# Kernel tuning notes

Measured on AMD Instinct MI355X. Metric: run time of the kernel, lower is better.

The kernel has to match this reference:

```python
import jax, jax.numpy as jnp
import numpy as np

FEATURE_SIZE = 128
STRIDE = 16
BASE_SIZE = 16
RATIOS = [0.5, 1, 2]
SCALES = [8, 16, 32]


def _generate_anchors(feature_size, stride):
    # Faithful to the torch module's numpy anchor generation (incl. rounding).
    size = BASE_SIZE * BASE_SIZE
    size_ratios = size / np.array(RATIOS)
    ws = np.round(np.sqrt(size_ratios))
    hs = np.round(ws * np.array(RATIOS))
    base = []
    for w, h in zip(ws, hs):
        for s in SCALES:
            base.append([0.0, 0.0, w * s, h * s])
    base = np.array(base)  # [9, 4]
    xo, yo = np.meshgrid(np.arange(feature_size), np.arange(feature_size), indexing='ij')
    # original loop order: x outer, y inner, then 9 base anchors
    centers = np.stack([xo * stride, yo * stride], axis=-1).reshape(-1, 1, 2)  # [F*F,1,2]
    wh = np.broadcast_to(base[None, :, 2:4], (feature_size * feature_size, 9, 2))
    anchors = np.concatenate([np.broadcast_to(centers, wh.shape), wh], axis=-1).reshape(-1, 4)
    return jnp.asarray(anchors, dtype=jnp.float32)  # [F*F*9, 4]


def _conv(x, w, b, pad):
    y = jax.lax.conv_general_dilated(
        x, w, window_strides=(1, 1), padding=[(pad, pad), (pad, pad)],
        dimension_numbers=('NCHW', 'OIHW', 'NCHW'))
    return y + b[None, :, None, None]


def setup_inputs() -> dict:
    key = jax.random.key(0)
    ks = jax.random.split(key, 4)
    F = FEATURE_SIZE
    x = jax.random.normal(ks[0], (1, 1024, F, F), dtype=jnp.float32)
    base_w = jax.random.normal(ks[1], (512, 1024, 3, 3), dtype=jnp.float32) * 0.01
    base_b = jnp.zeros((512,), dtype=jnp.float32)
    cls_w = jax.random.normal(ks[2], (18, 512, 1, 1), dtype=jnp.float32) * 0.01
    cls_b = jnp.zeros((18,), dtype=jnp.float32)
    reg_w = jax.random.normal(ks[3], (36, 512, 1, 1), dtype=jnp.float32) * 0.01
    reg_b = jnp.zeros((36,), dtype=jnp.float32)
    return {"x": x, "base_w": base_w, "base_b": base_b,
            "cls_w": cls_w, "cls_b": cls_b, "reg_w": reg_w, "reg_b": reg_b}


def reference(x, base_w, base_b, cls_w, cls_b, reg_w, reg_b):
    F = FEATURE_SIZE
    anchors = _generate_anchors(F, STRIDE)  # [N,4], N = F*F*9

    rpn_conv = jax.nn.relu(_conv(x, base_w, base_b, pad=1))        # [1,512,F,F]
    rpn_cls = _conv(rpn_conv, cls_w, cls_b, pad=0)                  # [1,18,F,F]
    # softmax over the 2-way fg/bg axis after reshape, as in the original
    cls_rs = rpn_cls.reshape(1, 2, 9 * F, F)
    cls_prob = jax.nn.softmax(cls_rs, axis=1).reshape(1, 18, F, F)
    rpn_reg = _conv(rpn_conv, reg_w, reg_b, pad=0)                  # [1,36,F,F]

    cls = jnp.transpose(cls_prob, (0, 2, 3, 1)).reshape(-1, 2)      # [N,2]
    reg = jnp.transpose(rpn_reg, (0, 2, 3, 1)).reshape(-1, 4)       # [N,4]

    # Vectorized decode — faithful to the original per-anchor loop math:
    # p0 = ax + aw*d0 ; p1 = ay + ah*d1 ; p2 = aw + exp(d2) ; p3 = ah + exp(d3)
    p0 = anchors[:, 0] + anchors[:, 2] * reg[:, 0]
    p1 = anchors[:, 1] + anchors[:, 3] * reg[:, 1]
    p2 = anchors[:, 2] + jnp.exp(reg[:, 2])
    p3 = anchors[:, 3] + jnp.exp(reg[:, 3])
    proposals = jnp.stack([p0, p1, p2, p3], axis=-1)                # [N,4]
    scores = cls[:, 1]                                              # [N]
    return jnp.concatenate([proposals, scores[:, None]], axis=-1)   # [N,5]
```

## Files before the change

kernel.cpp:

```cpp
#include <hip/hip_runtime.h>
#include <hip/hip_bf16.h>

typedef unsigned short u16;
typedef short s8v __attribute__((ext_vector_type(8)));
typedef float f4v __attribute__((ext_vector_type(4)));

#define F 128
#define CIN 1024
#define CMID 512
#define XP 130
#define K9 9216
#define BK 64

__device__ __forceinline__ u16 f2bf(float v) {
    union { float f; unsigned u; } x; x.f = v;
    unsigned r = x.u + 0x7fff + ((x.u >> 16) & 1);
    return (u16)(r >> 16);
}
__device__ __forceinline__ float bf2f(u16 u) {
    union { unsigned u; float f; } x; x.u = ((unsigned)u) << 16; return x.f;
}

__device__ __forceinline__ void gl16(const u16* g, u16* l) {
    __builtin_amdgcn_global_load_lds(
        (const __attribute__((address_space(1))) void*)g,
        (__attribute__((address_space(3))) void*)l,
        16, 0, 0);
}

__constant__ float WBASE[9] = {184.f, 368.f, 736.f, 128.f, 256.f, 512.f,  88.f, 176.f, 352.f};
__constant__ float HBASE[9] = { 96.f, 192.f, 384.f, 128.f, 256.f, 512.f, 176.f, 352.f, 704.f};

__global__ void prep_border(u16* __restrict__ xpad) {
    int t = blockIdx.x * 256 + threadIdx.x;
    if (t >= 516 * 1024) return;
    int c = t & 1023;
    int cell = t >> 10;
    int h, w;
    if (cell < 130)      { h = 0;   w = cell; }
    else if (cell < 260) { h = 129; w = cell - 130; }
    else { int rm = cell - 260; h = 1 + (rm >> 1); w = (rm & 1) * 129; }
    xpad[(h * XP + w) * CIN + c] = 0;
}

__global__ void prep_xpad(const float* __restrict__ x, u16* __restrict__ xpad) {
    __shared__ float lds[64][65];
    const int h  = blockIdx.x;
    const int w0 = blockIdx.y * 64;
    const int c0 = blockIdx.z * 64;
    const int tid = threadIdx.x;
    {
        const int wl = tid & 63, ci = tid >> 6;
        #pragma unroll
        for (int k = 0; k < 16; ++k) {
            int cl = ci * 16 + k;
            lds[cl][wl] = x[(c0 + cl) * (F * F) + h * F + (w0 + wl)];
        }
    }
    __syncthreads();
    {
        const int cs = (tid & 7) * 8;
        #pragma unroll
        for (int pass = 0; pass < 2; ++pass) {
            const int wl = (tid >> 3) + pass * 32;
            s8v v;
            #pragma unroll
            for (int j = 0; j < 8; ++j) v[j] = (short)f2bf(lds[cs + j][wl]);
            *(s8v*)&xpad[((h + 1) * XP + (w0 + wl + 1)) * CIN + c0 + cs] = v;
        }
    }
}

__global__ void prep_wt(const float* __restrict__ bw, u16* __restrict__ wt) {
    __shared__ u16 lds[K9];
    const int oc = blockIdx.x;
    const int tid = threadIdx.x;
    for (int k = 0; k < 36; ++k) {
        int idx = k * 256 + tid;
        float v = bw[oc * K9 + idx];
        int c = idx / 9, q = idx - c * 9;
        lds[q * CIN + c] = f2bf(v);
    }
    __syncthreads();
    for (int k = 0; k < 36; ++k) {
        int idx = k * 256 + tid;
        wt[oc * K9 + idx] = lds[idx];
    }
}

__global__ void prep_wc(const float* __restrict__ cls_w, const float* __restrict__ reg_w,
                        u16* __restrict__ wc) {
    int t = blockIdx.x * 256 + threadIdx.x;
    int oc = t >> 9, c = t & 511;
    float v = 0.f;
    if (oc < 18)      v = cls_w[oc * 512 + c];
    else if (oc < 54) v = reg_w[(oc - 18) * 512 + c];
    wc[t] = f2bf(v);
}

__global__ __launch_bounds__(256, 2) void gemm_conv(
    const u16* __restrict__ xpad, const u16* __restrict__ wt,
    const float* __restrict__ bias, u16* __restrict__ rpn) {
    __shared__ u16 smem[4 * 128 * BK];
    const int tid = threadIdx.x;
    const int gh  = blockIdx.x;
    const int oc0 = blockIdx.y * 128;

    const int lane = tid & 63;
    const int wv = tid >> 6;
    const int lm = lane & 15;
    const int lq = lane >> 4;
    const int wm = (wv >> 1) * 64;
    const int wn = (wv & 1) * 64;

    const u16* pa[4];
    const u16* pb[4];
    #pragma unroll
    for (int j = 0; j < 4; ++j) {
        int r = wv * 32 + j * 8 + (lane >> 3);
        int s8 = ((lane & 7) ^ (r & 7)) * 8;
        pa[j] = xpad + r * CIN + s8;
        pb[j] = wt + (size_t)(oc0 + r) * K9 + s8;
    }

    f4v acc[4][4] = {};

    auto issue = [&](int step, int buf) {
        const int dydx = step >> 4;
        const int cc   = step & 15;
        const int dy = dydx / 3, dx = dydx - dy * 3;
        const int aoff = ((gh + dy) * XP + dx) * CIN + cc * 64;
        const int boff = dydx * CIN + cc * 64;
        u16* Ab = smem + (buf * 2 + 0) * (128 * BK) + (wv * 32) * BK;
        u16* Bb = smem + (buf * 2 + 1) * (128 * BK) + (wv * 32) * BK;
        #pragma unroll
        for (int j = 0; j < 4; ++j) {
            gl16(pa[j] + aoff, Ab + j * 8 * BK);
            gl16(pb[j] + boff, Bb + j * 8 * BK);
        }
    };

    issue(0, 0);
    __syncthreads();
    for (int step = 0; step < 144; ++step) {
        const int buf = step & 1;
        if (step + 1 < 144) issue(step + 1, buf ^ 1);
        const u16* Ab = smem + (buf * 2 + 0) * (128 * BK);
        const u16* Bb = smem + (buf * 2 + 1) * (128 * BK);
        #pragma unroll
        for (int kk = 0; kk < 2; ++kk) {
            s8v af[4], bfr[4];
            #pragma unroll
            for (int i = 0; i < 4; ++i) {
                int ra = wm + i * 16 + lm;
                int rb = wn + i * 16 + lm;
                af[i]  = *(const s8v*)&Ab[ra * BK + (((kk * 4 + lq) ^ (ra & 7)) * 8)];
                bfr[i] = *(const s8v*)&Bb[rb * BK + (((kk * 4 + lq) ^ (rb & 7)) * 8)];
            }
            #pragma unroll
            for (int mi = 0; mi < 4; ++mi)
                #pragma unroll
                for (int ni = 0; ni < 4; ++ni)
                    acc[mi][ni] = __builtin_amdgcn_mfma_f32_16x16x32_bf16(
                        af[mi], bfr[ni], acc[mi][ni], 0, 0, 0);
        }
        __syncthreads();
    }

    #pragma unroll
    for (int ni = 0; ni < 4; ++ni) {
        const int oc = oc0 + wn + ni * 16 + lm;
        const float b = bias[oc];
        #pragma unroll
        for (int mi = 0; mi < 4; ++mi) {
            #pragma unroll
            for (int rr = 0; rr < 4; ++rr) {
                const int m = wm + mi * 16 + lq * 4 + rr;
                float v = acc[mi][ni][rr] + b;
                v = v > 0.f ? v : 0.f;
                rpn[(gh * 128 + m) * CMID + oc] = f2bf(v);
            }
        }
    }
}

__global__ __launch_bounds__(256) void stage2(
    const u16* __restrict__ rpn, const u16* __restrict__ wc,
    const float* __restrict__ cls_b, const float* __restrict__ reg_b,
    float* __restrict__ vals) {
    const int tid = threadIdx.x, lane = tid & 63, wv = tid >> 6;
    const int lm = lane & 15, lq = lane >> 4;
    const int m0 = blockIdx.x * 64 + wv * 16;
    f4v acc[4] = {};
    const u16* arow = rpn + (m0 + lm) * CMID + lq * 8;
    const u16* brow = wc + lm * CMID + lq * 8;
    #pragma unroll
    for (int k = 0; k < 16; ++k) {
        s8v af = *(const s8v*)(arow + k * 32);
        #pragma unroll
        for (int ni = 0; ni < 4; ++ni) {
            s8v bf = *(const s8v*)(brow + ni * 16 * CMID + k * 32);
            acc[ni] = __builtin_amdgcn_mfma_f32_16x16x32_bf16(af, bf, acc[ni], 0, 0, 0);
        }
    }
    #pragma unroll
    for (int ni = 0; ni < 4; ++ni) {
        const int ch = ni * 16 + lm;
        const float b = ch < 18 ? cls_b[ch] : (ch < 54 ? reg_b[ch - 18] : 0.f);
        #pragma unroll
        for (int rr = 0; rr < 4; ++rr)
            vals[(m0 + lq * 4 + rr) * 64 + ch] = acc[ni][rr] + b;
    }
}

__global__ void stage3(const float* __restrict__ vals, float* __restrict__ out) {
    const int t = blockIdx.x * 256 + threadIdx.x;
    const int p = t / 9, a = t - p * 9;
    const float* v = vals + p * 64;
    const int ch = 2 * a + 1;
    const int pair = (ch < 9) ? ch + 9 : ch - 9;
    const float score = 1.f / (1.f + expf(v[pair] - v[ch]));
    const float r0 = v[18 + 4 * a], r1 = v[19 + 4 * a];
    const float r2 = v[20 + 4 * a], r3 = v[21 + 4 * a];
    const float wb = WBASE[a], hb = HBASE[a];
    const int h = p >> 7, w = p & 127;
    float* o = out + t * 5;
    o[0] = h * 16.f + wb * r0;
    o[1] = w * 16.f + hb * r1;
    o[2] = wb + expf(r2);
    o[3] = hb + expf(r3);
    o[4] = score;
}

extern "C" void kernel_launch(void* const* d_in, const int* in_sizes, int n_in,
                              void* d_out, int out_size, void* d_ws, size_t ws_size,
                              hipStream_t stream) {
    const float* x      = (const float*)d_in[0];
    const float* base_w = (const float*)d_in[1];
    const float* base_b = (const float*)d_in[2];
    const float* cls_w  = (const float*)d_in[3];
    const float* cls_b  = (const float*)d_in[4];
    const float* reg_w  = (const float*)d_in[5];
    const float* reg_b  = (const float*)d_in[6];
    float* out = (float*)d_out;

    char* ws = (char*)d_ws;
    u16*  xpad = (u16*)ws;
    u16*  wt   = (u16*)(ws + 34611200);
    u16*  wc   = (u16*)(ws + 34611200 + 9437184);
    u16*  rpn  = (u16*)(ws + 34611200 + 9437184 + 65536);
    float* vals = (float*)(ws + 34611200 + 9437184 + 65536 + 16777216);

    prep_border<<<2064, 256, 0, stream>>>(xpad);
    prep_xpad<<<dim3(128, 2, 16), 256, 0, stream>>>(x, xpad);
    prep_wt<<<512, 256, 0, stream>>>(base_w, wt);
    prep_wc<<<128, 256, 0, stream>>>(cls_w, reg_w, wc);
    gemm_conv<<<dim3(128, 4), 256, 0, stream>>>(xpad, wt, base_b, rpn);
    stage2<<<256, 256, 0, stream>>>(rpn, wc, cls_b, reg_b, vals);
    stage3<<<576, 256, 0, stream>>>(vals, out);
}
```

Measured before the change: 278.7 us.

## Merge prep kernels, share A tile across dx taps, fuse stage2 and stage3

Merges the four preprocessing kernels into a single launch, with vectorized border zeroing and a padded LDS stride for the weight transpose. The conv GEMM now loads a 130-row A tile once per (dy, channel-chunk) and reuses it for all three dx taps by shifting row indices, so only B is reloaded per step. Block indices are remapped so that neighbouring rows and output-channel tiles run close together, which may improve L2 reuse. The 1x1 conv and decode stages are fused through shared memory, which removes the intermediate vals buffer and one launch. The cost is a more complex pipeline with an extra sync per dx step and slightly more LDS use.

```diff
diff --git a/kernel.cpp b/kernel.cpp
--- a/kernel.cpp
+++ b/kernel.cpp
@@ -10,7 +10,11 @@
 #define CMID 512
 #define XP 130
 #define K9 9216
-#define BK 64
+
+#define A_ELEMS 8704
+#define B_ELEMS 8192
+#define AOFF(b) ((b) * A_ELEMS)
+#define BOFF(b) (2 * A_ELEMS + (b) * B_ELEMS)
 
 __device__ __forceinline__ u16 f2bf(float v) {
     union { float f; unsigned u; } x; x.f = v;
@@ -31,80 +35,82 @@
 __constant__ float WBASE[9] = {184.f, 368.f, 736.f, 128.f, 256.f, 512.f,  88.f, 176.f, 352.f};
 __constant__ float HBASE[9] = { 96.f, 192.f, 384.f, 128.f, 256.f, 512.f, 176.f, 352.f, 704.f};
 
-__global__ void prep_border(u16* __restrict__ xpad) {
-    int t = blockIdx.x * 256 + threadIdx.x;
-    if (t >= 516 * 1024) return;
-    int c = t & 1023;
-    int cell = t >> 10;
-    int h, w;
-    if (cell < 130)      { h = 0;   w = cell; }
-    else if (cell < 260) { h = 129; w = cell - 130; }
-    else { int rm = cell - 260; h = 1 + (rm >> 1); w = (rm & 1) * 129; }
-    xpad[(h * XP + w) * CIN + c] = 0;
-}
-
-__global__ void prep_xpad(const float* __restrict__ x, u16* __restrict__ xpad) {
-    __shared__ float lds[64][65];
-    const int h  = blockIdx.x;
-    const int w0 = blockIdx.y * 64;
-    const int c0 = blockIdx.z * 64;
+__global__ __launch_bounds__(256) void prep_all(
+    const float* __restrict__ x, const float* __restrict__ bw,
+    const float* __restrict__ cls_w, const float* __restrict__ reg_w,
+    u16* __restrict__ xpad, u16* __restrict__ wt, u16* __restrict__ wc) {
+    __shared__ char ldsraw[18624];
+    const int b = blockIdx.x;
     const int tid = threadIdx.x;
-    {
-        const int wl = tid & 63, ci = tid >> 6;
-        #pragma unroll
-        for (int k = 0; k < 16; ++k) {
-            int cl = ci * 16 + k;
-            lds[cl][wl] = x[(c0 + cl) * (F * F) + h * F + (w0 + wl)];
-        }
-    }
-    __syncthreads();
-    {
-        const int cs = (tid & 7) * 8;
-        #pragma unroll
-        for (int pass = 0; pass < 2; ++pass) {
-            const int wl = (tid >> 3) + pass * 32;
-            s8v v;
-            #pragma unroll
-            for (int j = 0; j < 8; ++j) v[j] = (short)f2bf(lds[cs + j][wl]);
-            *(s8v*)&xpad[((h + 1) * XP + (w0 + wl + 1)) * CIN + c0 + cs] = v;
-        }
-    }
-}
-
-__global__ void prep_wt(const float* __restrict__ bw, u16* __restrict__ wt) {
-    __shared__ u16 lds[K9];
-    const int oc = blockIdx.x;
-    const int tid = threadIdx.x;
-    for (int k = 0; k < 36; ++k) {
-        int idx = k * 256 + tid;
-        float v = bw[oc * K9 + idx];
-        int c = idx / 9, q = idx - c * 9;
-        lds[q * CIN + c] = f2bf(v);
-    }
-    __syncthreads();
-    for (int k = 0; k < 36; ++k) {
-        int idx = k * 256 + tid;
-        wt[oc * K9 + idx] = lds[idx];
-    }
-}
-
-__global__ void prep_wc(const float* __restrict__ cls_w, const float* __restrict__ reg_w,
-                        u16* __restrict__ wc) {
-    int t = blockIdx.x * 256 + threadIdx.x;
-    int oc = t >> 9, c = t & 511;
-    float v = 0.f;
-    if (oc < 18)      v = cls_w[oc * 512 + c];
-    else if (oc < 54) v = reg_w[(oc - 18) * 512 + c];
-    wc[t] = f2bf(v);
+
+    if (b < 258) {
+        int t = b * 256 + tid;
+        int cell = t >> 7, c8 = (t & 127) * 8;
+        int h, w;
+        if (cell < 130)      { h = 0;   w = cell; }
+        else if (cell < 260) { h = 129; w = cell - 130; }
+        else { int rm = cell - 260; h = 1 + (rm >> 1); w = (rm & 1) * 129; }
+        s8v z = {};
+        *(s8v*)&xpad[(h * XP + w) * CIN + c8] = z;
+    } else if (b < 4354) {
+        float (*lds)[65] = (float(*)[65])ldsraw;
+        const int b2 = b - 258;
+        const int h  = b2 >> 5;
+        const int w0 = ((b2 >> 4) & 1) * 64;
+        const int c0 = (b2 & 15) * 64;
+        {
+            const int wl = tid & 63, ci = tid >> 6;
+            #pragma unroll
+            for (int k = 0; k < 16; ++k) {
+                int cl = ci * 16 + k;
+                lds[cl][wl] = x[(c0 + cl) * (F * F) + h * F + (w0 + wl)];
+            }
+        }
+        __syncthreads();
+        {
+            const int cs = (tid & 7) * 8;
+            #pragma unroll
+            for (int pass = 0; pass < 2; ++pass) {
+                const int wl = (tid >> 3) + pass * 32;
+                s8v v;
+                #pragma unroll
+                for (int j = 0; j < 8; ++j) v[j] = (short)f2bf(lds[cs + j][wl]);
+                *(s8v*)&xpad[((h + 1) * XP + (w0 + wl + 1)) * CIN + c0 + cs] = v;
+            }
+        }
+    } else if (b < 4866) {
+        u16* lds = (u16*)ldsraw;
+        const int oc = b - 4354;
+        for (int k = 0; k < 36; ++k) {
+            int idx = k * 256 + tid;
+            float v = bw[oc * K9 + idx];
+            int c = idx / 9, q = idx - c * 9;
+            lds[q * 1033 + c] = f2bf(v);
+        }
+        __syncthreads();
+        for (int k = 0; k < 36; ++k) {
+            int idx = k * 256 + tid;
+            int q = idx >> 10, c = idx & 1023;
+            wt[oc * K9 + idx] = lds[q * 1033 + c];
+        }
+    } else {
+        int t = (b - 4866) * 256 + tid;
+        int oc = t >> 9, c = t & 511;
+        float v = 0.f;
+        if (oc < 18)      v = cls_w[oc * 512 + c];
+        else if (oc < 54) v = reg_w[(oc - 18) * 512 + c];
+        wc[t] = f2bf(v);
+    }
 }
 
 __global__ __launch_bounds__(256, 2) void gemm_conv(
     const u16* __restrict__ xpad, const u16* __restrict__ wt,
     const float* __restrict__ bias, u16* __restrict__ rpn) {
-    __shared__ u16 smem[4 * 128 * BK];
+    __shared__ u16 smem[2 * A_ELEMS + 2 * B_ELEMS];
     const int tid = threadIdx.x;
-    const int gh  = blockIdx.x;
-    const int oc0 = blockIdx.y * 128;
+    const int bid = blockIdx.x;
+    const int oc0 = ((bid & 7) >> 1) * 128;
+    const int gh  = (bid >> 3) * 2 + (bid & 1);
 
     const int lane = tid & 63;
     const int wv = tid >> 6;
@@ -113,70 +119,81 @@
     const int wm = (wv >> 1) * 64;
     const int wn = (wv & 1) * 64;
 
-    const u16* pa[4];
-    const u16* pb[4];
-    #pragma unroll
-    for (int j = 0; j < 4; ++j) {
-        int r = wv * 32 + j * 8 + (lane >> 3);
-        int s8 = ((lane & 7) ^ (r & 7)) * 8;
-        pa[j] = xpad + r * CIN + s8;
-        pb[j] = wt + (size_t)(oc0 + r) * K9 + s8;
-    }
+    const int sw = (lane & 7) ^ ((lane >> 3) & 7);
+    const u16* pA = xpad + (lane >> 3) * CIN + sw * 8;
+    const u16* pB = wt + (size_t)(oc0 + wv * 32 + (lane >> 3)) * K9 + sw * 8;
 
     f4v acc[4][4] = {};
 
-    auto issue = [&](int step, int buf) {
-        const int dydx = step >> 4;
-        const int cc   = step & 15;
-        const int dy = dydx / 3, dx = dydx - dy * 3;
-        const int aoff = ((gh + dy) * XP + dx) * CIN + cc * 64;
-        const int boff = dydx * CIN + cc * 64;
-        u16* Ab = smem + (buf * 2 + 0) * (128 * BK) + (wv * 32) * BK;
-        u16* Bb = smem + (buf * 2 + 1) * (128 * BK) + (wv * 32) * BK;
-        #pragma unroll
-        for (int j = 0; j < 4; ++j) {
-            gl16(pa[j] + aoff, Ab + j * 8 * BK);
-            gl16(pb[j] + boff, Bb + j * 8 * BK);
-        }
+    auto issueA = [&](int ms) {
+        const int dy = ms >> 4, cc = ms & 15;
+        const u16* src = pA + ((gh + dy) * XP) * CIN + cc * 64;
+        u16* dst = &smem[AOFF(ms & 1)];
+        #pragma unroll
+        for (int jj = 0; jj < 4; ++jj) {
+            const int ci = wv * 4 + jj;
+            gl16(src + ci * 8 * CIN, dst + ci * 512);
+        }
+        if (wv == 0) gl16(src + 16 * 8 * CIN, dst + 16 * 512);
     };
-
-    issue(0, 0);
+    auto issueB = [&](int ms, int dx, int buf) {
+        const int dy = ms >> 4, cc = ms & 15;
+        const int dydx = dy * 3 + dx;
+        const u16* src = pB + dydx * CIN + cc * 64;
+        u16* dst = &smem[BOFF(buf) + wv * 32 * 64];
+        #pragma unroll
+        for (int jj = 0; jj < 4; ++jj)
+            gl16(src + jj * 8 * K9, dst + jj * 8 * 64);
+    };
+
+    issueA(0);
+    issueB(0, 0, 0);
     __syncthreads();
-    for (int step = 0; step < 144; ++step) {
-        const int buf = step & 1;
-        if (step + 1 < 144) issue(step + 1, buf ^ 1);
-        const u16* Ab = smem + (buf * 2 + 0) * (128 * BK);
-        const u16* Bb = smem + (buf * 2 + 1) * (128 * BK);
-        #pragma unroll
-        for (int kk = 0; kk < 2; ++kk) {
-            s8v af[4], bfr[4];
-            #pragma unroll
-            for (int i = 0; i < 4; ++i) {
-                int ra = wm + i * 16 + lm;
-                int rb = wn + i * 16 + lm;
-                af[i]  = *(const s8v*)&Ab[ra * BK + (((kk * 4 + lq) ^ (ra & 7)) * 8)];
-                bfr[i] = *(const s8v*)&Bb[rb * BK + (((kk * 4 + lq) ^ (rb & 7)) * 8)];
-            }
-            #pragma unroll
-            for (int mi = 0; mi < 4; ++mi)
+
+    int t = 0;
+    for (int ms = 0; ms < 48; ++ms) {
+        const u16* Ab = &smem[AOFF(ms & 1)];
+        #pragma unroll
+        for (int dx = 0; dx < 3; ++dx, ++t) {
+            if (t + 1 < 144) {
+                const int msn = (dx == 2) ? ms + 1 : ms;
+                const int dxn = (dx == 2) ? 0 : dx + 1;
+                issueB(msn, dxn, (t + 1) & 1);
+            }
+            if (dx == 0 && ms + 1 < 48) issueA(ms + 1);
+            const u16* Bb = &smem[BOFF(t & 1)];
+            #pragma unroll
+            for (int kk = 0; kk < 2; ++kk) {
+                const int kseg = kk * 4 + lq;
+                s8v af[4], bfr[4];
                 #pragma unroll
-                for (int ni = 0; ni < 4; ++ni)
-                    acc[mi][ni] = __builtin_amdgcn_mfma_f32_16x16x32_bf16(
-                        af[mi], bfr[ni], acc[mi][ni], 0, 0, 0);
-        }
-        __syncthreads();
+                for (int i = 0; i < 4; ++i) {
+                    const int ra = wm + i * 16 + lm + dx;
+                    const int rb = wn + i * 16 + lm;
+                    af[i]  = *(const s8v*)&Ab[ra * 64 + ((kseg ^ (ra & 7)) << 3)];
+                    bfr[i] = *(const s8v*)&Bb[rb * 64 + ((kseg ^ (rb & 7)) << 3)];
+                }
+                #pragma unroll
+                for (int mi = 0; mi < 4; ++mi)
+                    #pragma unroll
+                    for (int ni = 0; ni < 4; ++ni)
+                        acc[mi][ni] = __builtin_amdgcn_mfma_f32_16x16x32_bf16(
+                            af[mi], bfr[ni], acc[mi][ni], 0, 0, 0);
+            }
+            __syncthreads();
+        }
     }
 
     #pragma unroll
     for (int ni = 0; ni < 4; ++ni) {
         const int oc = oc0 + wn + ni * 16 + lm;
-        const float b = bias[oc];
+        const float bv = bias[oc];
         #pragma unroll
         for (int mi = 0; mi < 4; ++mi) {
             #pragma unroll
             for (int rr = 0; rr < 4; ++rr) {
                 const int m = wm + mi * 16 + lq * 4 + rr;
-                float v = acc[mi][ni][rr] + b;
+                float v = acc[mi][ni][rr] + bv;
                 v = v > 0.f ? v : 0.f;
                 rpn[(gh * 128 + m) * CMID + oc] = f2bf(v);
             }
@@ -184,10 +201,11 @@
     }
 }
 
-__global__ __launch_bounds__(256) void stage2(
+__global__ __launch_bounds__(256) void stage23(
     const u16* __restrict__ rpn, const u16* __restrict__ wc,
     const float* __restrict__ cls_b, const float* __restrict__ reg_b,
-    float* __restrict__ vals) {
+    float* __restrict__ out) {
+    __shared__ float vals[64][65];
     const int tid = threadIdx.x, lane = tid & 63, wv = tid >> 6;
     const int lm = lane & 15, lq = lane >> 4;
     const int m0 = blockIdx.x * 64 + wv * 16;
@@ -206,30 +224,31 @@
     #pragma unroll
     for (int ni = 0; ni < 4; ++ni) {
         const int ch = ni * 16 + lm;
-        const float b = ch < 18 ? cls_b[ch] : (ch < 54 ? reg_b[ch - 18] : 0.f);
+        const float bv = ch < 18 ? cls_b[ch] : (ch < 54 ? reg_b[ch - 18] : 0.f);
         #pragma unroll
         for (int rr = 0; rr < 4; ++rr)
-            vals[(m0 + lq * 4 + rr) * 64 + ch] = acc[ni][rr] + b;
-    }
-}
-
-__global__ void stage3(const float* __restrict__ vals, float* __restrict__ out) {
-    const int t = blockIdx.x * 256 + threadIdx.x;
-    const int p = t / 9, a = t - p * 9;
-    const float* v = vals + p * 64;
-    const int ch = 2 * a + 1;
-    const int pair = (ch < 9) ? ch + 9 : ch - 9;
-    const float score = 1.f / (1.f + expf(v[pair] - v[ch]));
-    const float r0 = v[18 + 4 * a], r1 = v[19 + 4 * a];
-    const float r2 = v[20 + 4 * a], r3 = v[21 + 4 * a];
-    const float wb = WBASE[a], hb = HBASE[a];
-    const int h = p >> 7, w = p & 127;
-    float* o = out + t * 5;
-    o[0] = h * 16.f + wb * r0;
-    o[1] = w * 16.f + hb * r1;
-    o[2] = wb + expf(r2);
-    o[3] = hb + expf(r3);
-    o[4] = score;
+            vals[wv * 16 + lq * 4 + rr][ch] = acc[ni][rr] + bv;
+    }
+    __syncthreads();
+    const int pbase = blockIdx.x * 64;
+    for (int q = tid; q < 576; q += 256) {
+        const int pl = q / 9, a = q - pl * 9;
+        const float* v = vals[pl];
+        const int ch = 2 * a + 1;
+        const int pair = (ch < 9) ? ch + 9 : ch - 9;
+        const float score = 1.f / (1.f + expf(v[pair] - v[ch]));
+        const float r0 = v[18 + 4 * a], r1 = v[19 + 4 * a];
+        const float r2 = v[20 + 4 * a], r3 = v[21 + 4 * a];
+        const float wb = WBASE[a], hb = HBASE[a];
+        const int p = pbase + pl;
+        const int h = p >> 7, w = p & 127;
+        float* o = out + (p * 9 + a) * 5;
+        o[0] = h * 16.f + wb * r0;
+        o[1] = w * 16.f + hb * r1;
+        o[2] = wb + expf(r2);
+        o[3] = hb + expf(r3);
+        o[4] = score;
+    }
 }
 
 extern "C" void kernel_launch(void* const* d_in, const int* in_sizes, int n_in,
@@ -245,17 +264,12 @@
     float* out = (float*)d_out;
 
     char* ws = (char*)d_ws;
-    u16*  xpad = (u16*)ws;
-    u16*  wt   = (u16*)(ws + 34611200);
-    u16*  wc   = (u16*)(ws + 34611200 + 9437184);
-    u16*  rpn  = (u16*)(ws + 34611200 + 9437184 + 65536);
-    float* vals = (float*)(ws + 34611200 + 9437184 + 65536 + 16777216);
-
-    prep_border<<<2064, 256, 0, stream>>>(xpad);
-    prep_xpad<<<dim3(128, 2, 16), 256, 0, stream>>>(x, xpad);
-    prep_wt<<<512, 256, 0, stream>>>(base_w, wt);
-    prep_wc<<<128, 256, 0, stream>>>(cls_w, reg_w, wc);
-    gemm_conv<<<dim3(128, 4), 256, 0, stream>>>(xpad, wt, base_b, rpn);
-    stage2<<<256, 256, 0, stream>>>(rpn, wc, cls_b, reg_b, vals);
-    stage3<<<576, 256, 0, stream>>>(vals, out);
-}
+    u16* xpad = (u16*)ws;
+    u16* wt   = (u16*)(ws + 34611200);
+    u16* wc   = (u16*)(ws + 34611200 + 9437184);
+    u16* rpn  = (u16*)(ws + 34611200 + 9437184 + 65536);
+
+    prep_all<<<4994, 256, 0, stream>>>(x, base_w, cls_w, reg_w, xpad, wt, wc);
+    gemm_conv<<<512, 256, 0, stream>>>(xpad, wt, base_b, rpn);
+    stage23<<<256, 256, 0, stream>>>(rpn, wc, cls_b, reg_b, out);
+}
```

New measurement: 276.4 us. Within noise of the previous version (-0.8%).
